# Kernel optimization log

Hardware: AMD Instinct MI355X
Metric: run time of the kernel (lower is better)

## Reference

```python
import jax, jax.numpy as jnp
import numpy as np

VAR_NUM, IN_DIM, OUT_DIM = 3, 8, 32
N_PTS, M_PTS, K_LAST = 8192, 2048, 10
RADIUS = 0.0342
PROJ_HIDDEN = 64
N_DIM = 2
MLP_DIMS = [2 * N_DIM + OUT_DIM, 80, 80, OUT_DIM]  # [36, 80, 80, 32]


def _gelu(x):
    # torch F.gelu default = exact erf form
    return jax.nn.gelu(x, approximate=False)


def _radius_neighbors(data, queries, r):
    # CSR-style neighbor lists (indices grouped per query), chunked for memory
    idx_chunks = []
    counts = np.zeros(queries.shape[0], np.int64)
    r2 = r * r
    for s in range(0, queries.shape[0], 1024):
        q = queries[s:s + 1024]
        d2 = ((q[:, None, :] - data[None, :, :]) ** 2).sum(-1)
        mask = d2 <= r2
        _, cols = np.nonzero(mask)  # row-major -> grouped by query
        idx_chunks.append(cols.astype(np.int32))
        counts[s:s + q.shape[0]] = mask.sum(1)
    return np.concatenate(idx_chunks), counts.astype(np.int32)


def _knn(data, queries, k):
    out = np.zeros((queries.shape[0], k), np.int32)
    for s in range(0, queries.shape[0], 1024):
        q = queries[s:s + 1024]
        d2 = ((q[:, None, :] - data[None, :, :]) ** 2).sum(-1)
        out[s:s + q.shape[0]] = np.argpartition(d2, k, axis=1)[:, :k]
    return out.reshape(-1)


def _mlp_params(key, dims):
    Ws, bs = [], []
    for i in range(len(dims) - 1):
        key, k1 = jax.random.split(key)
        Ws.append(jax.random.normal(k1, (dims[i], dims[i + 1]), jnp.float32) / np.sqrt(dims[i]).astype(np.float32))
        bs.append(jnp.zeros((dims[i + 1],), jnp.float32))
    return Ws, bs


def setup_inputs():
    rng = np.random.default_rng(0)
    input_grid = rng.uniform(size=(N_PTS, N_DIM)).astype(np.float32)
    output_grid = rng.uniform(size=(M_PTS, N_DIM)).astype(np.float32)
    nbr_index, nbr_counts = _radius_neighbors(input_grid, input_grid, RADIUS)
    nbr_seg = np.repeat(np.arange(N_PTS, dtype=np.int32), nbr_counts)
    nbr_last_index = _knn(input_grid, output_grid, K_LAST)

    key = jax.random.key(0)
    ks = jax.random.split(key, 4)
    inp = jax.random.normal(ks[0], (1, N_PTS, VAR_NUM * IN_DIM), jnp.float32)
    pW, pb = _mlp_params(ks[1], [IN_DIM, PROJ_HIDDEN, OUT_DIM])
    it0_W, it0_b = _mlp_params(ks[2], MLP_DIMS)
    it1_W, it1_b = _mlp_params(ks[3], MLP_DIMS)
    return dict(
        inp=inp,
        input_grid=jnp.asarray(input_grid), output_grid=jnp.asarray(output_grid),
        proj_W0=pW[0], proj_b0=pb[0], proj_W1=pW[1], proj_b1=pb[1],
        it0_W0=it0_W[0], it0_b0=it0_b[0], it0_W1=it0_W[1], it0_b1=it0_b[1], it0_W2=it0_W[2], it0_b2=it0_b[2],
        it1_W0=it1_W[0], it1_b0=it1_b[0], it1_W1=it1_W[1], it1_b1=it1_b[1], it1_W2=it1_W[2], it1_b2=it1_b[2],
        nbr_index=jnp.asarray(nbr_index), nbr_seg=jnp.asarray(nbr_seg),
        nbr_counts=jnp.asarray(nbr_counts), nbr_last_index=jnp.asarray(nbr_last_index),
    )


def _mlp3(x, W0, b0, W1, b1, W2, b2):
    x = _gelu(x @ W0 + b0)
    x = _gelu(x @ W1 + b1)
    return x @ W2 + b2


def reference(inp, input_grid, output_grid, proj_W0, proj_b0, proj_W1, proj_b1,
              it0_W0, it0_b0, it0_W1, it0_b1, it0_W2, it0_b2,
              it1_W0, it1_b0, it1_W1, it1_b1, it1_W2, it1_b2,
              nbr_index, nbr_seg, nbr_counts, nbr_last_index):
    B, N, _ = inp.shape  # B must be 1 (module's IT indexing assumes it)
    x = inp.reshape(B * N, VAR_NUM, IN_DIM)
    # pointwise projection MLP (gelu between layers)
    x = _gelu(x @ proj_W0 + proj_b0) @ proj_W1 + proj_b1  # (N, V, OUT_DIM)

    inv_counts = (1.0 / jnp.maximum(nbr_counts, 1).astype(x.dtype))[:, None]
    y_pos = input_grid[nbr_index]        # (E, 2) neighbor positions
    self_pos = input_grid[nbr_seg]       # (E, 2) query positions
    last_y = input_grid[nbr_last_index]                    # (M*K, 2)
    last_self = jnp.repeat(output_grid, K_LAST, axis=0)    # (M*K, 2)

    outs = []
    for v in range(VAR_NUM):
        f = x[:, v, :]
        # IT layer 0: radius neighborhoods on input grid, residual add
        agg = jnp.concatenate([y_pos, self_pos, f[nbr_index]], axis=-1)  # (E, 36)
        h = _mlp3(agg, it0_W0, it0_b0, it0_W1, it0_b1, it0_W2, it0_b2)
        f = jax.ops.segment_sum(h, nbr_seg, num_segments=N) * inv_counts + f
        # IT layer 1 (last): fixed-K neighbors from input grid to output grid, mean
        agg = jnp.concatenate([last_y, last_self, f[nbr_last_index]], axis=-1)
        h = _mlp3(agg, it1_W0, it1_b0, it1_W1, it1_b1, it1_W2, it1_b2)
        outs.append(h.reshape(M_PTS, K_LAST, OUT_DIM).mean(axis=1))
    # original concatenates temp[None] along dim=2 -> (1, M, V*OUT_DIM)
    return jnp.concatenate(outs, axis=-1)[None]
```

## Files before the change

### kernel.cpp

```cpp
#include <hip/hip_runtime.h>
#include <hip/hip_bf16.h>
#include <math.h>

#define N_PTS 8192
#define M_PTS 2048
#define KLAST 10
#define VARS 3
#define OUTD 32
#define D1 80
#define D2 80
#define PB 16
#define LPTS 4
#define NT 768
#define NWAVES 12
#define TPCH 104
#define W0P 72
#define W1P 104
#define RP 40

typedef float f4 __attribute__((ext_vector_type(4)));
typedef short bf16x8 __attribute__((ext_vector_type(8)));

__device__ __forceinline__ float gelu_f(float x) {
    float x2 = x * x;
    float t = x * (0.7978845608028654f + 0.0356774081f * x2);
    float u = __expf(2.0f * t);
    float th = 1.0f - 2.0f * __builtin_amdgcn_rcpf(u + 1.0f);
    return 0.5f * x * (1.0f + th);
}
__device__ __forceinline__ unsigned short f2bf(float x) {
    unsigned int u = __float_as_uint(x);
    u += 0x7FFF + ((u >> 16) & 1);
    return (unsigned short)(u >> 16);
}
__device__ __forceinline__ float bf2f(unsigned short h) {
    return __uint_as_float(((unsigned int)h) << 16);
}
__device__ __forceinline__ int pk2(float a, float b) {
    __hip_bfloat162 h = __float22bfloat162_rn(float2{a, b});
    int r; __builtin_memcpy(&r, &h, 4); return r;
}

__device__ __forceinline__ void stage_weights(
    unsigned short* W0h, unsigned short* W1h, unsigned short* W2h, float* bs,
    const float* __restrict__ W0g, const float* __restrict__ b0g,
    const float* __restrict__ W1g, const float* __restrict__ b1g,
    const float* __restrict__ W2g, const float* __restrict__ b2g, int t)
{
    for (int idx = t; idx < D1 * W0P; idx += NT) {
        int col = idx / W0P, k = idx - col * W0P;
        float w = (k < 32) ? W0g[(k + 4) * D1 + col]
                           : ((k < 36) ? W0g[(k - 32) * D1 + col] : 0.0f);
        W0h[idx] = f2bf(w);
    }
    for (int idx = t; idx < D1 * W1P; idx += NT) {
        int col = idx / W1P, k = idx - col * W1P;
        W1h[idx] = f2bf((k < D2) ? W1g[k * D1 + col] : 0.0f);
    }
    for (int idx = t; idx < OUTD * W1P; idx += NT) {
        int col = idx / W1P, k = idx - col * W1P;
        W2h[idx] = f2bf((k < D2) ? W2g[k * OUTD + col] : 0.0f);
    }
    for (int idx = t; idx < 192; idx += NT)
        bs[idx] = (idx < 80) ? b0g[idx] : (idx < 160 ? b1g[idx - 80] : b2g[idx - 160]);
}

__device__ __forceinline__ void mlp_chunk(
    int4 featsi, int4 posfi, unsigned short* Trow,
    const unsigned short* W0h, const unsigned short* W1h,
    const unsigned short* W2h, const float* bs, int lm, int quad)
{
    bf16x8 b1f0 = *(bf16x8*)&featsi;
    bf16x8 b1f1 = *(bf16x8*)&posfi;
#pragma unroll 1
    for (int cb = 0; cb < 5; ++cb) {
        f4 acc = *(const f4*)&bs[cb * 16 + quad * 4];
        bf16x8 a0 = *(const bf16x8*)&W0h[(cb * 16 + lm) * W0P + quad * 8];
        bf16x8 a1 = *(const bf16x8*)&W0h[(cb * 16 + lm) * W0P + 32 + quad * 8];
        acc = __builtin_amdgcn_mfma_f32_16x16x32_bf16(a0, b1f0, acc, 0, 0, 0);
        acc = __builtin_amdgcn_mfma_f32_16x16x32_bf16(a1, b1f1, acc, 0, 0, 0);
        *(int2*)&Trow[cb * 16 + quad * 4] =
            make_int2(pk2(gelu_f(acc.x), gelu_f(acc.y)),
                      pk2(gelu_f(acc.z), gelu_f(acc.w)));
    }
    bf16x8 b2f[3];
    b2f[0] = *(const bf16x8*)&Trow[quad * 8];
    b2f[1] = *(const bf16x8*)&Trow[32 + quad * 8];
    b2f[2] = *(const bf16x8*)&Trow[64 + quad * 8];
#pragma unroll 1
    for (int cb = 0; cb < 5; ++cb) {
        f4 acc = *(const f4*)&bs[80 + cb * 16 + quad * 4];
        const unsigned short* wh = &W1h[(cb * 16 + lm) * W1P + quad * 8];
        bf16x8 h0 = *(const bf16x8*)&wh[0];
        bf16x8 h1 = *(const bf16x8*)&wh[32];
        bf16x8 h2 = *(const bf16x8*)&wh[64];
        acc = __builtin_amdgcn_mfma_f32_16x16x32_bf16(h0, b2f[0], acc, 0, 0, 0);
        acc = __builtin_amdgcn_mfma_f32_16x16x32_bf16(h1, b2f[1], acc, 0, 0, 0);
        acc = __builtin_amdgcn_mfma_f32_16x16x32_bf16(h2, b2f[2], acc, 0, 0, 0);
        *(int2*)&Trow[cb * 16 + quad * 4] =
            make_int2(pk2(gelu_f(acc.x), gelu_f(acc.y)),
                      pk2(gelu_f(acc.z), gelu_f(acc.w)));
    }
    bf16x8 b3f[3];
    b3f[0] = *(const bf16x8*)&Trow[quad * 8];
    b3f[1] = *(const bf16x8*)&Trow[32 + quad * 8];
    b3f[2] = *(const bf16x8*)&Trow[64 + quad * 8];
    float* po = (float*)Trow;
#pragma unroll 1
    for (int cb = 0; cb < 2; ++cb) {
        f4 acc = *(const f4*)&bs[160 + cb * 16 + quad * 4];
        const unsigned short* wh = &W2h[(cb * 16 + lm) * W1P + quad * 8];
        bf16x8 h0 = *(const bf16x8*)&wh[0];
        bf16x8 h1 = *(const bf16x8*)&wh[32];
        bf16x8 h2 = *(const bf16x8*)&wh[64];
        acc = __builtin_amdgcn_mfma_f32_16x16x32_bf16(h0, b3f[0], acc, 0, 0, 0);
        acc = __builtin_amdgcn_mfma_f32_16x16x32_bf16(h1, b3f[1], acc, 0, 0, 0);
        acc = __builtin_amdgcn_mfma_f32_16x16x32_bf16(h2, b3f[2], acc, 0, 0, 0);
        *(f4*)&po[cb * 16 + quad * 4] = acc;
    }
}

__global__ __launch_bounds__(1024) void scan_kernel(
    const int* __restrict__ counts, int* __restrict__ offsets)
{
    __shared__ int wtot[16], wexc[16];
    const int t = threadIdx.x, lane = t & 63, wave = t >> 6;
    int4 a = ((const int4*)counts)[2 * t];
    int4 b = ((const int4*)counts)[2 * t + 1];
    int e1 = a.x, e2 = e1 + a.y, e3 = e2 + a.z, e4 = e3 + a.w;
    int e5 = e4 + b.x, e6 = e5 + b.y, e7 = e6 + b.z;
    int s = e7 + b.w;
    int x = s;
#pragma unroll
    for (int d = 1; d < 64; d <<= 1) {
        int y = __shfl_up(x, d);
        if (lane >= d) x += y;
    }
    if (lane == 63) wtot[wave] = x;
    int lane_base = x - s;
    __syncthreads();
    if (wave == 0 && lane < 16) {
        int v = wtot[lane];
        int xx = v;
#pragma unroll
        for (int d = 1; d < 16; d <<= 1) {
            int y = __shfl_up(xx, d);
            if (lane >= d) xx += y;
        }
        wexc[lane] = xx - v;
    }
    __syncthreads();
    int base = wexc[wave] + lane_base;
    ((int4*)offsets)[2 * t]     = make_int4(base, base + e1, base + e2, base + e3);
    ((int4*)offsets)[2 * t + 1] = make_int4(base + e4, base + e5, base + e6, base + e7);
}

__global__ __launch_bounds__(256) void proj_kernel(
    const float* __restrict__ inp, const float* __restrict__ grid_in,
    const float* __restrict__ W0, const float* __restrict__ b0,
    const float* __restrict__ W1, const float* __restrict__ b1,
    unsigned short* __restrict__ f0b)
{
    __shared__ float W0s[8 * 64];
    __shared__ float W1s[64 * OUTD];
    __shared__ float xs[32 * 8];
    __shared__ float H[32 * 64];
    const int t = threadIdx.x;
    const int r0 = blockIdx.x * 32;
    for (int idx = t; idx < 512; idx += 256) W0s[idx] = W0[idx];
    for (int idx = t; idx < 64 * OUTD; idx += 256) W1s[idx] = W1[idx];
    xs[t] = inp[r0 * 8 + t];
    if (t < 32) {
        int row = r0 + t, n = row / 3, v = row - n * 3;
        *(int*)(f0b + ((size_t)(v << 13) + n) * RP + 32) =
            pk2(grid_in[2 * n], grid_in[2 * n + 1]);
    }
    __syncthreads();
#pragma unroll 1
    for (int p = 0; p < 8; ++p) {
        int o = t + 256 * p, r = o >> 6, col = o & 63;
        float s = b0[col];
#pragma unroll
        for (int k = 0; k < 8; ++k) s += xs[r * 8 + k] * W0s[k * 64 + col];
        H[o] = gelu_f(s);
    }
    __syncthreads();
#pragma unroll 1
    for (int p = 0; p < 4; ++p) {
        int o = t + 256 * p, r = o >> 5, c = o & 31;
        float s = b1[c];
#pragma unroll 8
        for (int k = 0; k < 64; ++k) s += H[r * 64 + k] * W1s[k * OUTD + c];
        int row = r0 + r;
        int n = row / 3, v = row - n * 3;
        f0b[((size_t)(v << 13) + n) * RP + c] = f2bf(s);
    }
}

__global__ __launch_bounds__(768, 6) void agg_kernel(
    const float* __restrict__ grid_in, const unsigned short* __restrict__ f0b,
    const int* __restrict__ nbr_index, const int* __restrict__ offsets,
    const int* __restrict__ counts,
    const float* __restrict__ W0g, const float* __restrict__ b0g,
    const float* __restrict__ W1g, const float* __restrict__ b1g,
    const float* __restrict__ W2g, const float* __restrict__ b2g,
    unsigned short* __restrict__ f1b)
{
    __shared__ __attribute__((aligned(16))) unsigned short Tb[NWAVES * 16 * TPCH];
    __shared__ __attribute__((aligned(16))) unsigned short W0h[D1 * W0P];
    __shared__ __attribute__((aligned(16))) unsigned short W1h[D1 * W1P];
    __shared__ __attribute__((aligned(16))) unsigned short W2h[OUTD * W1P];
    __shared__ __attribute__((aligned(16))) float bs[192];
    __shared__ __attribute__((aligned(16))) float accH[VARS * PB * 32];
    __shared__ int offs[PB + 1];
    __shared__ int px2b[PB];
    __shared__ float invb[PB];

    const int t = threadIdx.x;
    const int lane = t & 63, wave = t >> 6;
    const int lm = lane & 15, quad = lane >> 4;
    const int p0 = blockIdx.x * PB;

    stage_weights(W0h, W1h, W2h, bs, W0g, b0g, W1g, b1g, W2g, b2g, t);
    if (t < PB) {
        offs[t] = offsets[p0 + t];
        int c = counts[p0 + t];
        invb[t] = 1.0f / (float)(c > 1 ? c : 1);
        px2b[t] = pk2(grid_in[2 * (p0 + t)], grid_in[2 * (p0 + t) + 1]);
    }
    if (t == PB) offs[PB] = offsets[p0 + PB - 1] + counts[p0 + PB - 1];
    for (int idx = t; idx < VARS * PB * 32; idx += NT) accH[idx] = 0.0f;
    __syncthreads();

    unsigned short* TbW = Tb + (wave * 16) * TPCH;
    if (lane < 32)
        *(int4*)(TbW + (lane >> 1) * TPCH + 80 + (lane & 1) * 8) = make_int4(0, 0, 0, 0);

    const int e0 = offs[0];
    const int cntT = offs[PB] - e0;
    const int Rb = VARS * cntT;
    const int nch = (Rb + 15) >> 4;

    unsigned short* Trow = TbW + lm * TPCH;

    int pkey; int4 pfeats, pposf;
    {
        int myrow = (wave << 4) + lm;
        pkey = -1; pfeats = make_int4(0,0,0,0); pposf = make_int4(0,0,0,0);
        if (myrow < Rb) {
            int myv = (myrow >= 2 * cntT) ? 2 : ((myrow >= cntT) ? 1 : 0);
            int e = e0 + myrow - myv * cntT;
            int myj = nbr_index[e];
            int lp = 0;
#pragma unroll
            for (int l = 1; l < PB; ++l) lp += (e >= offs[l]);
            pkey = myv * PB + lp;
            const unsigned short* rec = f0b + ((size_t)(myv << 13) + myj) * RP;
            pfeats = ((const int4*)rec)[quad];
            if (quad == 0) pposf = make_int4(*(const int*)(rec + 32), px2b[lp], 0, 0);
        }
    }

    for (int ch = wave; ch < nch; ch += NWAVES) {
        int ckey = pkey; int4 cfeats = pfeats, cposf = pposf;
        int nc = ch + NWAVES;
        pkey = -1; pfeats = make_int4(0,0,0,0); pposf = make_int4(0,0,0,0);
        if (nc < nch) {
            int myrow = (nc << 4) + lm;
            if (myrow < Rb) {
                int myv = (myrow >= 2 * cntT) ? 2 : ((myrow >= cntT) ? 1 : 0);
                int e = e0 + myrow - myv * cntT;
                int myj = nbr_index[e];
                int lp = 0;
#pragma unroll
                for (int l = 1; l < PB; ++l) lp += (e >= offs[l]);
                pkey = myv * PB + lp;
                const unsigned short* rec = f0b + ((size_t)(myv << 13) + myj) * RP;
                pfeats = ((const int4*)rec)[quad];
                if (quad == 0) pposf = make_int4(*(const int*)(rec + 32), px2b[lp], 0, 0);
            }
        }
        if (ckey < 0) { cfeats = make_int4(0,0,0,0); cposf = make_int4(0,0,0,0); }
        mlp_chunk(cfeats, cposf, Trow, W0h, W1h, W2h, bs, lm, quad);
        int col = lane & 31, eo = lane >> 5;
#pragma unroll 1
        for (int e2 = eo; e2 < 16; e2 += 2) {
            int k = __shfl(ckey, e2);
            if (k >= 0)
                atomicAdd(&accH[k * 32 + col], ((const float*)(TbW + e2 * TPCH))[col]);
        }
    }
    __syncthreads();
    for (int idx = t; idx < VARS * PB * OUTD; idx += NT) {
        int key = idx >> 5, c = idx & 31;
        int v = key >> 4, lp = key & 15;
        size_t rec = ((size_t)(v << 13) + p0 + lp) * RP;
        float val = accH[key * 32 + c] * invb[lp] + bf2f(f0b[rec + c]);
        f1b[rec + c] = f2bf(val);
    }
    if (t < VARS * PB) {
        int v = t >> 4, lp = t & 15;
        *(int*)(f1b + ((size_t)(v << 13) + p0 + lp) * RP + 32) = px2b[lp];
    }
}

__global__ __launch_bounds__(768, 6) void last_kernel(
    const unsigned short* __restrict__ f1b, const float* __restrict__ grid_out,
    const int* __restrict__ nbr_last,
    const float* __restrict__ W0g, const float* __restrict__ b0g,
    const float* __restrict__ W1g, const float* __restrict__ b1g,
    const float* __restrict__ W2g, const float* __restrict__ b2g,
    float* __restrict__ out)
{
    __shared__ __attribute__((aligned(16))) unsigned short Tb[NWAVES * 16 * TPCH];
    __shared__ __attribute__((aligned(16))) unsigned short W0h[D1 * W0P];
    __shared__ __attribute__((aligned(16))) unsigned short W1h[D1 * W1P];
    __shared__ __attribute__((aligned(16))) unsigned short W2h[OUTD * W1P];
    __shared__ __attribute__((aligned(16))) float bs[192];
    __shared__ __attribute__((aligned(16))) float accH[LPTS * VARS * 32];
    __shared__ int pxo2b[LPTS];

    const int t = threadIdx.x;
    const int lane = t & 63, wave = t >> 6;
    const int lm = lane & 15, quad = lane >> 4;
    const int m0 = blockIdx.x * LPTS;

    stage_weights(W0h, W1h, W2h, bs, W0g, b0g, W1g, b1g, W2g, b2g, t);
    if (t < LPTS)
        pxo2b[t] = pk2(grid_out[2 * (m0 + t)], grid_out[2 * (m0 + t) + 1]);
    for (int idx = t; idx < LPTS * VARS * 32; idx += NT) accH[idx] = 0.0f;
    __syncthreads();
    unsigned short* TbW = Tb + (wave * 16) * TPCH;
    if (lane < 32)
        *(int4*)(TbW + (lane >> 1) * TPCH + 80 + (lane & 1) * 8) = make_int4(0, 0, 0, 0);

    const int Rb = LPTS * VARS * KLAST;
    const int nch = (Rb + 15) >> 4;
    unsigned short* Trow = TbW + lm * TPCH;

    for (int ch = wave; ch < nch; ch += NWAVES) {
        int myrow = (ch << 4) + lm;
        int ckey = -1; int4 cfeats = make_int4(0,0,0,0), cposf = make_int4(0,0,0,0);
        if (myrow < Rb) {
            int lp = myrow / 30, rr = myrow - lp * 30;
            int v = rr / KLAST, kk = rr - v * KLAST;
            int myj = nbr_last[(m0 + lp) * KLAST + kk];
            ckey = lp * VARS + v;
            const unsigned short* rec = f1b + ((size_t)(v << 13) + myj) * RP;
            cfeats = ((const int4*)rec)[quad];
            if (quad == 0) cposf = make_int4(*(const int*)(rec + 32), pxo2b[lp], 0, 0);
        }
        mlp_chunk(cfeats, cposf, Trow, W0h, W1h, W2h, bs, lm, quad);
        int col = lane & 31, eo = lane >> 5;
#pragma unroll 1
        for (int e2 = eo; e2 < 16; e2 += 2) {
            int k = __shfl(ckey, e2);
            if (k >= 0)
                atomicAdd(&accH[k * 32 + col], ((const float*)(TbW + e2 * TPCH))[col]);
        }
    }
    __syncthreads();
    if (t < LPTS * VARS * OUTD) {
        int key = t >> 5, c = t & 31;
        int lp = key / VARS, v = key - lp * VARS;
        out[((size_t)(m0 + lp) * VARS + v) * OUTD + c] = accH[key * 32 + c] * (1.0f / KLAST);
    }
}

extern "C" void kernel_launch(void* const* d_in, const int* in_sizes, int n_in,
                              void* d_out, int out_size, void* d_ws, size_t ws_size,
                              hipStream_t stream) {
    const float* inp      = (const float*)d_in[0];
    const float* grid_in  = (const float*)d_in[1];
    const float* grid_out = (const float*)d_in[2];
    const float* pW0 = (const float*)d_in[3];
    const float* pb0 = (const float*)d_in[4];
    const float* pW1 = (const float*)d_in[5];
    const float* pb1 = (const float*)d_in[6];
    const float* i0W0 = (const float*)d_in[7];
    const float* i0b0 = (const float*)d_in[8];
    const float* i0W1 = (const float*)d_in[9];
    const float* i0b1 = (const float*)d_in[10];
    const float* i0W2 = (const float*)d_in[11];
    const float* i0b2 = (const float*)d_in[12];
    const float* i1W0 = (const float*)d_in[13];
    const float* i1b0 = (const float*)d_in[14];
    const float* i1W1 = (const float*)d_in[15];
    const float* i1b1 = (const float*)d_in[16];
    const float* i1W2 = (const float*)d_in[17];
    const float* i1b2 = (const float*)d_in[18];
    const int* nbr_index  = (const int*)d_in[19];
    const int* nbr_counts = (const int*)d_in[21];
    const int* nbr_last   = (const int*)d_in[22];

    unsigned short* f0b = (unsigned short*)d_ws;
    unsigned short* f1b = f0b + (size_t)VARS * N_PTS * RP;
    int* offsets = (int*)(f1b + (size_t)VARS * N_PTS * RP);

    proj_kernel<<<(N_PTS * VARS) / 32, 256, 0, stream>>>(inp, grid_in, pW0, pb0, pW1, pb1, f0b);
    scan_kernel<<<1, 1024, 0, stream>>>(nbr_counts, offsets);
    agg_kernel<<<N_PTS / PB, NT, 0, stream>>>(grid_in, f0b, nbr_index, offsets, nbr_counts,
                                              i0W0, i0b0, i0W1, i0b1, i0W2, i0b2, f1b);
    last_kernel<<<M_PTS / LPTS, NT, 0, stream>>>(f1b, grid_out, nbr_last,
                                                 i1W0, i1b0, i1W1, i1b1, i1W2, i1b2,
                                                 (float*)d_out);
}
```

Baseline: 338.1 us.

## Accumulate MLP outputs directly from MFMA registers and simplify GELU and segment lookup

The final MLP layer now atomically adds its MFMA accumulator values straight into a padded (stride 33) shared accumulator. This replaces writing outputs to an LDS tile and then re-reading them with shuffles before the atomic adds. GELU is rewritten with exp2 and fused FMAs into an algebraically equivalent tanh form. Each edge's local point index now comes from nbr_seg instead of a 15-way compare loop against the offsets. The W2 pad is shrunk to 96, trading an extra global load per edge and more scattered LDS atomics for less LDS traffic and fewer ALU instructions.

After: 375.0 us. 1.11x slower.

```diff
diff --git a/kernel.cpp b/kernel.cpp
--- a/kernel.cpp
+++ b/kernel.cpp
@@ -16,6 +16,7 @@
 #define TPCH 104
 #define W0P 72
 #define W1P 104
+#define W2P 96
 #define RP 40
 
 typedef float f4 __attribute__((ext_vector_type(4)));
@@ -23,10 +24,10 @@
 
 __device__ __forceinline__ float gelu_f(float x) {
     float x2 = x * x;
-    float t = x * (0.7978845608028654f + 0.0356774081f * x2);
-    float u = __expf(2.0f * t);
-    float th = 1.0f - 2.0f * __builtin_amdgcn_rcpf(u + 1.0f);
-    return 0.5f * x * (1.0f + th);
+    float s = x * __builtin_fmaf(0.1029418f, x2, 2.3022083f);
+    float u = __builtin_amdgcn_exp2f(s);
+    float r = __builtin_amdgcn_rcpf(u + 1.0f);
+    return __builtin_fmaf(-x, r, x);
 }
 __device__ __forceinline__ unsigned short f2bf(float x) {
     unsigned int u = __float_as_uint(x);
@@ -57,8 +58,8 @@
         int col = idx / W1P, k = idx - col * W1P;
         W1h[idx] = f2bf((k < D2) ? W1g[k * D1 + col] : 0.0f);
     }
-    for (int idx = t; idx < OUTD * W1P; idx += NT) {
-        int col = idx / W1P, k = idx - col * W1P;
+    for (int idx = t; idx < OUTD * W2P; idx += NT) {
+        int col = idx / W2P, k = idx - col * W2P;
         W2h[idx] = f2bf((k < D2) ? W2g[k * OUTD + col] : 0.0f);
     }
     for (int idx = t; idx < 192; idx += NT)
@@ -68,7 +69,8 @@
 __device__ __forceinline__ void mlp_chunk(
     int4 featsi, int4 posfi, unsigned short* Trow,
     const unsigned short* W0h, const unsigned short* W1h,
-    const unsigned short* W2h, const float* bs, int lm, int quad)
+    const unsigned short* W2h, const float* bs,
+    float* accH, int ckey, int lm, int quad)
 {
     bf16x8 b1f0 = *(bf16x8*)&featsi;
     bf16x8 b1f1 = *(bf16x8*)&posfi;
@@ -105,18 +107,23 @@
     b3f[0] = *(const bf16x8*)&Trow[quad * 8];
     b3f[1] = *(const bf16x8*)&Trow[32 + quad * 8];
     b3f[2] = *(const bf16x8*)&Trow[64 + quad * 8];
-    float* po = (float*)Trow;
 #pragma unroll 1
     for (int cb = 0; cb < 2; ++cb) {
         f4 acc = *(const f4*)&bs[160 + cb * 16 + quad * 4];
-        const unsigned short* wh = &W2h[(cb * 16 + lm) * W1P + quad * 8];
+        const unsigned short* wh = &W2h[(cb * 16 + lm) * W2P + quad * 8];
         bf16x8 h0 = *(const bf16x8*)&wh[0];
         bf16x8 h1 = *(const bf16x8*)&wh[32];
         bf16x8 h2 = *(const bf16x8*)&wh[64];
         acc = __builtin_amdgcn_mfma_f32_16x16x32_bf16(h0, b3f[0], acc, 0, 0, 0);
         acc = __builtin_amdgcn_mfma_f32_16x16x32_bf16(h1, b3f[1], acc, 0, 0, 0);
         acc = __builtin_amdgcn_mfma_f32_16x16x32_bf16(h2, b3f[2], acc, 0, 0, 0);
-        *(f4*)&po[cb * 16 + quad * 4] = acc;
+        if (ckey >= 0) {
+            float* a = &accH[ckey * 33 + cb * 16 + quad * 4];
+            atomicAdd(&a[0], acc.x);
+            atomicAdd(&a[1], acc.y);
+            atomicAdd(&a[2], acc.z);
+            atomicAdd(&a[3], acc.w);
+        }
     }
 }
 
@@ -199,8 +206,8 @@
 
 __global__ __launch_bounds__(768, 6) void agg_kernel(
     const float* __restrict__ grid_in, const unsigned short* __restrict__ f0b,
-    const int* __restrict__ nbr_index, const int* __restrict__ offsets,
-    const int* __restrict__ counts,
+    const int* __restrict__ nbr_index, const int* __restrict__ nbr_seg,
+    const int* __restrict__ offsets, const int* __restrict__ counts,
     const float* __restrict__ W0g, const float* __restrict__ b0g,
     const float* __restrict__ W1g, const float* __restrict__ b1g,
     const float* __restrict__ W2g, const float* __restrict__ b2g,
@@ -209,12 +216,12 @@
     __shared__ __attribute__((aligned(16))) unsigned short Tb[NWAVES * 16 * TPCH];
     __shared__ __attribute__((aligned(16))) unsigned short W0h[D1 * W0P];
     __shared__ __attribute__((aligned(16))) unsigned short W1h[D1 * W1P];
-    __shared__ __attribute__((aligned(16))) unsigned short W2h[OUTD * W1P];
+    __shared__ __attribute__((aligned(16))) unsigned short W2h[OUTD * W2P];
     __shared__ __attribute__((aligned(16))) float bs[192];
-    __shared__ __attribute__((aligned(16))) float accH[VARS * PB * 32];
-    __shared__ int offs[PB + 1];
+    __shared__ __attribute__((aligned(16))) float accH[VARS * PB * 33];
     __shared__ int px2b[PB];
     __shared__ float invb[PB];
+    __shared__ int sE0, sCnt;
 
     const int t = threadIdx.x;
     const int lane = t & 63, wave = t >> 6;
@@ -223,21 +230,24 @@
 
     stage_weights(W0h, W1h, W2h, bs, W0g, b0g, W1g, b1g, W2g, b2g, t);
     if (t < PB) {
-        offs[t] = offsets[p0 + t];
         int c = counts[p0 + t];
         invb[t] = 1.0f / (float)(c > 1 ? c : 1);
         px2b[t] = pk2(grid_in[2 * (p0 + t)], grid_in[2 * (p0 + t) + 1]);
     }
-    if (t == PB) offs[PB] = offsets[p0 + PB - 1] + counts[p0 + PB - 1];
-    for (int idx = t; idx < VARS * PB * 32; idx += NT) accH[idx] = 0.0f;
+    if (t == PB) {
+        int e0 = offsets[p0];
+        sE0 = e0;
+        sCnt = offsets[p0 + PB - 1] + counts[p0 + PB - 1] - e0;
+    }
+    for (int idx = t; idx < VARS * PB * 33; idx += NT) accH[idx] = 0.0f;
     __syncthreads();
 
     unsigned short* TbW = Tb + (wave * 16) * TPCH;
     if (lane < 32)
         *(int4*)(TbW + (lane >> 1) * TPCH + 80 + (lane & 1) * 8) = make_int4(0, 0, 0, 0);
 
-    const int e0 = offs[0];
-    const int cntT = offs[PB] - e0;
+    const int e0 = sE0;
+    const int cntT = sCnt;
     const int Rb = VARS * cntT;
     const int nch = (Rb + 15) >> 4;
 
@@ -251,9 +261,7 @@
             int myv = (myrow >= 2 * cntT) ? 2 : ((myrow >= cntT) ? 1 : 0);
             int e = e0 + myrow - myv * cntT;
             int myj = nbr_index[e];
-            int lp = 0;
-#pragma unroll
-            for (int l = 1; l < PB; ++l) lp += (e >= offs[l]);
+            int lp = nbr_seg[e] - p0;
             pkey = myv * PB + lp;
             const unsigned short* rec = f0b + ((size_t)(myv << 13) + myj) * RP;
             pfeats = ((const int4*)rec)[quad];
@@ -271,9 +279,7 @@
                 int myv = (myrow >= 2 * cntT) ? 2 : ((myrow >= cntT) ? 1 : 0);
                 int e = e0 + myrow - myv * cntT;
                 int myj = nbr_index[e];
-                int lp = 0;
-#pragma unroll
-                for (int l = 1; l < PB; ++l) lp += (e >= offs[l]);
+                int lp = nbr_seg[e] - p0;
                 pkey = myv * PB + lp;
                 const unsigned short* rec = f0b + ((size_t)(myv << 13) + myj) * RP;
                 pfeats = ((const int4*)rec)[quad];
@@ -281,21 +287,14 @@
             }
         }
         if (ckey < 0) { cfeats = make_int4(0,0,0,0); cposf = make_int4(0,0,0,0); }
-        mlp_chunk(cfeats, cposf, Trow, W0h, W1h, W2h, bs, lm, quad);
-        int col = lane & 31, eo = lane >> 5;
-#pragma unroll 1
-        for (int e2 = eo; e2 < 16; e2 += 2) {
-            int k = __shfl(ckey, e2);
-            if (k >= 0)
-                atomicAdd(&accH[k * 32 + col], ((const float*)(TbW + e2 * TPCH))[col]);
-        }
+        mlp_chunk(cfeats, cposf, Trow, W0h, W1h, W2h, bs, accH, ckey, lm, quad);
     }
     __syncthreads();
     for (int idx = t; idx < VARS * PB * OUTD; idx += NT) {
         int key = idx >> 5, c = idx & 31;
         int v = key >> 4, lp = key & 15;
         size_t rec = ((size_t)(v << 13) + p0 + lp) * RP;
-        float val = accH[key * 32 + c] * invb[lp] + bf2f(f0b[rec + c]);
+        float val = accH[key * 33 + c] * invb[lp] + bf2f(f0b[rec + c]);
         f1b[rec + c] = f2bf(val);
     }
     if (t < VARS * PB) {
@@ -315,9 +314,9 @@
     __shared__ __attribute__((aligned(16))) unsigned short Tb[NWAVES * 16 * TPCH];
     __shared__ __attribute__((aligned(16))) unsigned short W0h[D1 * W0P];
     __shared__ __attribute__((aligned(16))) unsigned short W1h[D1 * W1P];
-    __shared__ __attribute__((aligned(16))) unsigned short W2h[OUTD * W1P];
+    __shared__ __attribute__((aligned(16))) unsigned short W2h[OUTD * W2P];
     __shared__ __attribute__((aligned(16))) float bs[192];
-    __shared__ __attribute__((aligned(16))) float accH[LPTS * VARS * 32];
+    __shared__ __attribute__((aligned(16))) float accH[LPTS * VARS * 33];
     __shared__ int pxo2b[LPTS];
 
     const int t = threadIdx.x;
@@ -328,7 +327,7 @@
     stage_weights(W0h, W1h, W2h, bs, W0g, b0g, W1g, b1g, W2g, b2g, t);
     if (t < LPTS)
         pxo2b[t] = pk2(grid_out[2 * (m0 + t)], grid_out[2 * (m0 + t) + 1]);
-    for (int idx = t; idx < LPTS * VARS * 32; idx += NT) accH[idx] = 0.0f;
+    for (int idx = t; idx < LPTS * VARS * 33; idx += NT) accH[idx] = 0.0f;
     __syncthreads();
     unsigned short* TbW = Tb + (wave * 16) * TPCH;
     if (lane < 32)
@@ -350,20 +349,13 @@
             cfeats = ((const int4*)rec)[quad];
             if (quad == 0) cposf = make_int4(*(const int*)(rec + 32), pxo2b[lp], 0, 0);
         }
-        mlp_chunk(cfeats, cposf, Trow, W0h, W1h, W2h, bs, lm, quad);
-        int col = lane & 31, eo = lane >> 5;
-#pragma unroll 1
-        for (int e2 = eo; e2 < 16; e2 += 2) {
-            int k = __shfl(ckey, e2);
-            if (k >= 0)
-                atomicAdd(&accH[k * 32 + col], ((const float*)(TbW + e2 * TPCH))[col]);
-        }
+        mlp_chunk(cfeats, cposf, Trow, W0h, W1h, W2h, bs, accH, ckey, lm, quad);
     }
     __syncthreads();
     if (t < LPTS * VARS * OUTD) {
         int key = t >> 5, c = t & 31;
         int lp = key / VARS, v = key - lp * VARS;
-        out[((size_t)(m0 + lp) * VARS + v) * OUTD + c] = accH[key * 32 + c] * (1.0f / KLAST);
+        out[((size_t)(m0 + lp) * VARS + v) * OUTD + c] = accH[key * 33 + c] * (1.0f / KLAST);
     }
 }
 
@@ -390,6 +382,7 @@
     const float* i1W2 = (const float*)d_in[17];
     const float* i1b2 = (const float*)d_in[18];
     const int* nbr_index  = (const int*)d_in[19];
+    const int* nbr_seg    = (const int*)d_in[20];
     const int* nbr_counts = (const int*)d_in[21];
     const int* nbr_last   = (const int*)d_in[22];
 
@@ -399,7 +392,8 @@
 
     proj_kernel<<<(N_PTS * VARS) / 32, 256, 0, stream>>>(inp, grid_in, pW0, pb0, pW1, pb1, f0b);
     scan_kernel<<<1, 1024, 0, stream>>>(nbr_counts, offsets);
-    agg_kernel<<<N_PTS / PB, NT, 0, stream>>>(grid_in, f0b, nbr_index, offsets, nbr_counts,
+    agg_kernel<<<N_PTS / PB, NT, 0, stream>>>(grid_in, f0b, nbr_index, nbr_seg, offsets,
+                                              nbr_counts,
                                               i0W0, i0b0, i0W1, i0b1, i0W2, i0b2, f1b);
     last_kernel<<<M_PTS / LPTS, NT, 0, stream>>>(f1b, grid_out, nbr_last,
                                                  i1W0, i1b0, i1W1, i1b1, i1W2, i1b2,
```
